# Performance work log

Measured on AMD Instinct MI355X. Metric: run time of the kernel, lower is better.

Reference implementation:

```python
import jax, jax.numpy as jnp
import numpy as np

B, S, D, E = 2, 2048, 1024, 16  # batch, cutoff (seq), dmodel, n_experts


def setup_inputs() -> dict:
    key = jax.random.key(0)
    k = jax.random.split(key, 6)
    scale = 1.0 / np.sqrt(D)
    return {
        "x": jax.random.normal(k[0], (B, S, D), dtype=jnp.float32),
        "gate": jax.random.normal(k[1], (D, E), dtype=jnp.float32) * scale,
        "W1": jax.random.normal(k[2], (E, D, D), dtype=jnp.float32) * scale,  # lin1: Linear(dmodel, dmodel*E), split per expert
        "b1": jnp.zeros((E, D), dtype=jnp.float32),
        "W2": jax.random.normal(k[3], (E, D, D), dtype=jnp.float32) * scale,  # lin2: Linear(dmodel*E, dmodel), split per expert
        "b2": jnp.zeros((D,), dtype=jnp.float32),
        "topk": 256,
    }


def reference(x, gate, W1, b1, W2, b2, topk):
    # Expert-choice gating: softmax over the token (cutoff) axis per expert.
    logits = jnp.einsum("bsd,de->bse", x, gate)            # (B, S, E)
    probs = jax.nn.softmax(logits, axis=1)                  # softmax over tokens
    # Each expert selects its top-k tokens.
    g, idx = jax.lax.top_k(jnp.swapaxes(probs, 1, 2), topk)  # (B, E, k)
    # Gather selected tokens: (B, E, k, D)
    xin = jnp.take_along_axis(x[:, None, :, :], idx[..., None], axis=2)
    # Per-expert 2-layer FFN (hidden size = dmodel, per width = dmodel*n_experts)
    h = jax.nn.relu(jnp.einsum("bekd,edf->bekf", xin, W1) + b1[None, :, None, :])
    out = jnp.einsum("bekf,efd->bekd", h, W2) + b2           # (B, E, k, D)
    weighted = out * g[..., None]
    # Scatter-add back to token positions.
    y = jnp.zeros_like(x)
    b_idx = jnp.arange(x.shape[0])[:, None, None]            # (B, 1, 1)
    y = y.at[b_idx, idx].add(weighted)
    return y
```

## Files before the change

kernel.cpp:

```cpp
#include <hip/hip_runtime.h>
#include <stdint.h>
#include <math.h>

constexpr int CB = 2;
constexpr int CS = 2048;
constexpr int CD = 1024;
constexpr int CE = 16;
constexpr int CK = 256;

typedef short bf16x8 __attribute__((ext_vector_type(8)));
typedef float f32x4 __attribute__((ext_vector_type(4)));

typedef __attribute__((address_space(1))) const unsigned int gu32;
typedef __attribute__((address_space(3))) unsigned int lu32;

__device__ __forceinline__ void async16(const void* g, void* l) {
    __builtin_amdgcn_global_load_lds((gu32*)g, (lu32*)l, 16, 0, 0);
}

__device__ inline unsigned short f2bf(float f) {
    union { float f; uint32_t u; } v; v.f = f;
    uint32_t u = v.u;
    uint32_t r = (u + 0x7FFFu + ((u >> 16) & 1u)) >> 16;
    return (unsigned short)r;
}

__global__ void logits_kernel(const float* __restrict__ x,
                              const float* __restrict__ gate,
                              float* __restrict__ logits) {
    const int bs = blockIdx.x;
    const int l = threadIdx.x;
    const float* xr = x + (size_t)bs * CD;
    float acc[CE];
#pragma unroll
    for (int e = 0; e < CE; e++) acc[e] = 0.0f;
    for (int i = 0; i < CD / 64; i++) {
        const int d = i * 64 + l;
        const float xv = xr[d];
        const float* g = gate + (size_t)d * CE;
#pragma unroll
        for (int e = 0; e < CE; e++) acc[e] += xv * g[e];
    }
#pragma unroll
    for (int e = 0; e < CE; e++) {
        float v = acc[e];
#pragma unroll
        for (int o = 32; o > 0; o >>= 1) v += __shfl_down(v, o);
        if (l == 0) logits[(size_t)bs * CE + e] = v;
    }
}

__global__ void topk_kernel(const float* __restrict__ logits,
                            int* __restrict__ idx_out,
                            float* __restrict__ g_out) {
    const int be = blockIdx.x;
    const int b = be >> 4, e = be & 15;
    const int tid = threadIdx.x;
    const int lane = tid & 63, wid = tid >> 6;

    __shared__ float redf[4];
    __shared__ int hist[256];
    __shared__ int wsum[4];
    __shared__ int sh_bin, sh_rank;
    __shared__ int scnt, eqc;
    __shared__ int eqbuf[CS];

    float lv[8], p[8];
    unsigned int uv[8];
#pragma unroll
    for (int j = 0; j < 8; j++) {
        const int s = tid + j * 256;
        lv[j] = logits[((size_t)(b * CS + s)) * CE + e];
    }
    float m = lv[0];
#pragma unroll
    for (int j = 1; j < 8; j++) m = fmaxf(m, lv[j]);
#pragma unroll
    for (int o = 32; o > 0; o >>= 1) m = fmaxf(m, __shfl_down(m, o));
    if (lane == 0) redf[wid] = m;
    __syncthreads();
    m = fmaxf(fmaxf(redf[0], redf[1]), fmaxf(redf[2], redf[3]));
    __syncthreads();
    float lsum = 0.0f;
#pragma unroll
    for (int j = 0; j < 8; j++) {
        p[j] = expf(lv[j] - m);
        uv[j] = __float_as_uint(p[j]);
        lsum += p[j];
    }
#pragma unroll
    for (int o = 32; o > 0; o >>= 1) lsum += __shfl_down(lsum, o);
    if (lane == 0) redf[wid] = lsum;
    __syncthreads();
    const float total = redf[0] + redf[1] + redf[2] + redf[3];
    const float inv_total = 1.0f / total;

    unsigned int prefix = 0;
    int kneed = CK;
    for (int pass = 0; pass < 4; pass++) {
        const int shift = 24 - 8 * pass;
        __syncthreads();
        hist[tid] = 0;
        __syncthreads();
        const unsigned int hmask = (pass == 0) ? 0u : (0xFFFFFFFFu << (shift + 8));
#pragma unroll
        for (int j = 0; j < 8; j++)
            if ((uv[j] & hmask) == prefix)
                atomicAdd(&hist[(uv[j] >> shift) & 255], 1);
        __syncthreads();
        const int own = hist[tid];
        int s = own;
#pragma unroll
        for (int o = 1; o < 64; o <<= 1) {
            int t = __shfl_down(s, o);
            if (lane + o < 64) s += t;
        }
        if (lane == 0) wsum[wid] = s;
        __syncthreads();
        int above = 0;
        for (int ww = wid + 1; ww < 4; ww++) above += wsum[ww];
        const int incl = s + above;
        if (incl >= kneed && (incl - own) < kneed) {
            sh_bin = tid;
            sh_rank = kneed - (incl - own);
        }
        __syncthreads();
        prefix |= ((unsigned int)sh_bin) << shift;
        kneed = sh_rank;
    }
    const unsigned int v = prefix;
    const int quota = kneed;

    if (tid == 0) { scnt = 0; eqc = 0; }
    __syncthreads();
#pragma unroll
    for (int j = 0; j < 8; j++) {
        const int s = tid + j * 256;
        if (uv[j] > v) {
            const int pos = atomicAdd(&scnt, 1);
            idx_out[be * CK + pos] = s;
            g_out[be * CK + pos] = p[j] * inv_total;
        } else if (uv[j] == v) {
            const int pos = atomicAdd(&eqc, 1);
            eqbuf[pos] = s;
        }
    }
    __syncthreads();
    if (tid == 0) {
        const int cgt = scnt;
        const int n = eqc;
        const float gv = __uint_as_float(v) * inv_total;
        if (n > quota) {
            for (int i = 0; i < quota; i++) {
                int mn = i;
                for (int k2 = i + 1; k2 < n; k2++)
                    if (eqbuf[k2] < eqbuf[mn]) mn = k2;
                const int t2 = eqbuf[i]; eqbuf[i] = eqbuf[mn]; eqbuf[mn] = t2;
            }
        }
        for (int i = 0; i < quota; i++) {
            idx_out[be * CK + cgt + i] = eqbuf[i];
            g_out[be * CK + cgt + i] = gv;
        }
    }
}

__global__ void gather_kernel(const float* __restrict__ x,
                              const int* __restrict__ idx_ws,
                              unsigned short* __restrict__ xinbuf) {
    const int row = blockIdx.x;
    const int be = row >> 8;
    const int b = be >> 4;
    const int tok = idx_ws[row];
    const int c0 = threadIdx.x * 4;
    const f32x4 f = *(const f32x4*)(x + ((size_t)b * CS + tok) * CD + c0);
    union { unsigned short u[4]; uint2 v; } t;
    t.u[0] = f2bf(f[0]); t.u[1] = f2bf(f[1]); t.u[2] = f2bf(f[2]); t.u[3] = f2bf(f[3]);
    *(uint2*)(xinbuf + (size_t)row * CD + c0) = t.v;
}

__global__ __launch_bounds__(256)
void wt_kernel(const float* __restrict__ W, unsigned short* __restrict__ Wt) {
    const int kt = blockIdx.x, nt = blockIdx.y, e = blockIdx.z;
    const float* src = W + (size_t)e * CD * CD;
    unsigned short* dst = Wt + (size_t)e * CD * CD;
    const int tid = threadIdx.x;
    __shared__ unsigned short T[64 * 64];

    const int kr = tid >> 4;
    const int n4 = (tid & 15) << 2;
#pragma unroll
    for (int it = 0; it < 4; it++) {
        const int k = it * 16 + kr;
        const f32x4 v = *(const f32x4*)(src + (size_t)(kt * 64 + k) * CD + nt * 64 + n4);
        const int pp = k >> 4;
        const int klo = k & 15;
#pragma unroll
        for (int i = 0; i < 4; i++) {
            const int n = n4 + i;
            T[n * 64 + ((pp ^ ((n >> 2) & 3)) << 4) + klo] = f2bf(v[i]);
        }
    }
    __syncthreads();
    const int n = tid >> 2;
    const int pp = tid & 3;
    const int sw = pp ^ ((n >> 2) & 3);
    const uint4 a = *(const uint4*)&T[n * 64 + (sw << 4)];
    const uint4 b = *(const uint4*)&T[n * 64 + (sw << 4) + 8];
    unsigned short* drow = dst + (size_t)(nt * 64 + n) * CD + kt * 64 + pp * 16;
    *(uint4*)drow = a;
    *(uint4*)(drow + 8) = b;
}

template <int PHASE>
__global__ __launch_bounds__(256, 2)
void ffn_gemm(const unsigned short* __restrict__ Ain,
              const unsigned short* __restrict__ Wt,
              const float* __restrict__ bias,
              unsigned short* __restrict__ hout,
              const int* __restrict__ idx_ws,
              const float* __restrict__ g_ws,
              float* __restrict__ y) {
    const int mtile = blockIdx.x;
    const int ntile = blockIdx.y;
    const int z = blockIdx.z;
    const int e = z >> 1, b = z & 1;
    const int be = b * 16 + e;
    const int tid = threadIdx.x;
    const int w = tid >> 6, l = tid & 63;
    const int wm = w & 1, wn = w >> 1;
    const int quad = l >> 4, lr = l & 15;

    __shared__ __align__(16) unsigned short As[128 * 32];
    __shared__ __align__(16) unsigned short Bs[128 * 32];

    f32x4 acc[4][4];
    const f32x4 zz = {0.f, 0.f, 0.f, 0.f};
#pragma unroll
    for (int mi = 0; mi < 4; mi++)
#pragma unroll
        for (int ni = 0; ni < 4; ni++) acc[mi][ni] = zz;

    const int sr = l >> 2;
    const int sc = l & 3;
    const unsigned short* Abase = Ain + ((size_t)be * CK + mtile * 128) * CD;
    const unsigned short* Bbase = Wt + ((size_t)e * CD + ntile * 128) * CD;

    for (int k0 = 0; k0 < CD; k0 += 32) {
#pragma unroll
        for (int j = 0; j < 2; j++) {
            const int row = (w * 2 + j) * 16 + sr;
            const size_t goff = (size_t)row * CD + k0 + sc * 8;
            const int loff = (w * 2 + j) * 512 + l * 8;
            async16(Abase + goff, &As[loff]);
            async16(Bbase + goff, &Bs[loff]);
        }
        __syncthreads();

        bf16x8 af[4], bf[4];
#pragma unroll
        for (int mi = 0; mi < 4; mi++)
            af[mi] = *(const bf16x8*)&As[(wm * 64 + mi * 16 + lr) * 32 + quad * 8];
#pragma unroll
        for (int ni = 0; ni < 4; ni++)
            bf[ni] = *(const bf16x8*)&Bs[(wn * 64 + ni * 16 + lr) * 32 + quad * 8];
#pragma unroll
        for (int mi = 0; mi < 4; mi++)
#pragma unroll
            for (int ni = 0; ni < 4; ni++)
                acc[mi][ni] = __builtin_amdgcn_mfma_f32_16x16x32_bf16(
                    af[mi], bf[ni], acc[mi][ni], 0, 0, 0);
        __syncthreads();
    }

    const int gn_base = ntile * 128 + wn * 64;
    if (PHASE == 0) {
#pragma unroll
        for (int mi = 0; mi < 4; mi++)
#pragma unroll
            for (int r = 0; r < 4; r++) {
                const int slot = mtile * 128 + wm * 64 + mi * 16 + quad * 4 + r;
                unsigned short* outrow = hout + ((size_t)be * CK + slot) * CD;
#pragma unroll
                for (int ni = 0; ni < 4; ni++) {
                    const int col = gn_base + ni * 16 + lr;
                    float hv = acc[mi][ni][r] + bias[e * CD + col];
                    hv = fmaxf(hv, 0.0f);
                    outrow[col] = f2bf(hv);
                }
            }
    } else {
#pragma unroll
        for (int mi = 0; mi < 4; mi++)
#pragma unroll
            for (int r = 0; r < 4; r++) {
                const int slot = mtile * 128 + wm * 64 + mi * 16 + quad * 4 + r;
                const int tok = idx_ws[be * CK + slot];
                const float gval = g_ws[be * CK + slot];
                float* yrow = y + ((size_t)b * CS + tok) * CD;
#pragma unroll
                for (int ni = 0; ni < 4; ni++) {
                    const int col = gn_base + ni * 16 + lr;
                    const float val = (acc[mi][ni][r] + bias[col]) * gval;
                    atomicAdd(&yrow[col], val);
                }
            }
    }
}

extern "C" void kernel_launch(void* const* d_in, const int* in_sizes, int n_in,
                              void* d_out, int out_size, void* d_ws, size_t ws_size,
                              hipStream_t stream) {
    const float* x    = (const float*)d_in[0];
    const float* gate = (const float*)d_in[1];
    const float* W1   = (const float*)d_in[2];
    const float* b1   = (const float*)d_in[3];
    const float* W2   = (const float*)d_in[4];
    const float* b2   = (const float*)d_in[5];
    float* y = (float*)d_out;

    char* ws = (char*)d_ws;
    float* logits = (float*)ws;
    int* idxw = (int*)(ws + 262144);
    float* gw = (float*)(ws + 294912);
    unsigned short* xinbuf = (unsigned short*)(ws + 327680);
    unsigned short* hbuf = (unsigned short*)(ws + 17104896);
    unsigned short* wtbuf = (unsigned short*)(ws + 33882112);

    logits_kernel<<<CB * CS, 64, 0, stream>>>(x, gate, logits);
    topk_kernel<<<CB * CE, 256, 0, stream>>>(logits, idxw, gw);
    gather_kernel<<<CB * CE * CK, 256, 0, stream>>>(x, idxw, xinbuf);
    wt_kernel<<<dim3(16, 16, CE), 256, 0, stream>>>(W1, wtbuf);
    hipMemsetAsync(d_out, 0, (size_t)CB * CS * CD * sizeof(float), stream);
    ffn_gemm<0><<<dim3(2, 8, CB * CE), 256, 0, stream>>>(xinbuf, wtbuf, b1, hbuf, idxw, gw, y);
    wt_kernel<<<dim3(16, 16, CE), 256, 0, stream>>>(W2, wtbuf);
    ffn_gemm<1><<<dim3(2, 8, CB * CE), 256, 0, stream>>>(hbuf, wtbuf, b2, nullptr, idxw, gw, y);
}
```

Measured before the change: 302.8 us.

## Retile FFN GEMM to 128x64 with K=64 swizzled LDS, vectorize logits kernel

The FFN GEMM tile shrinks from 128x128 to 128x64 and the K step grows from 32 to 64. This doubles the grid to 1024 blocks and halves the number of barriers per K loop. LDS loads now use an XOR swizzle to avoid bank conflicts, and launch bounds rise to 4 blocks per CU for higher occupancy. The logits kernel packs 4 tokens per 256-thread block and uses vector float4 loads. The cost is less reuse of A per tile and more register pressure under the tighter launch bound.

```diff
diff --git a/kernel.cpp b/kernel.cpp
--- a/kernel.cpp
+++ b/kernel.cpp
@@ -25,21 +25,31 @@
     return (unsigned short)r;
 }
 
-__global__ void logits_kernel(const float* __restrict__ x,
-                              const float* __restrict__ gate,
-                              float* __restrict__ logits) {
-    const int bs = blockIdx.x;
-    const int l = threadIdx.x;
+__global__ __launch_bounds__(256)
+void logits_kernel(const float* __restrict__ x,
+                   const float* __restrict__ gate,
+                   float* __restrict__ logits) {
+    const int tid = threadIdx.x;
+    const int wid = tid >> 6, l = tid & 63;
+    const int bs = blockIdx.x * 4 + wid;
     const float* xr = x + (size_t)bs * CD;
     float acc[CE];
 #pragma unroll
     for (int e = 0; e < CE; e++) acc[e] = 0.0f;
-    for (int i = 0; i < CD / 64; i++) {
-        const int d = i * 64 + l;
-        const float xv = xr[d];
-        const float* g = gate + (size_t)d * CE;
-#pragma unroll
-        for (int e = 0; e < CE; e++) acc[e] += xv * g[e];
+#pragma unroll
+    for (int i = 0; i < 4; i++) {
+        const int d0 = i * 256 + l * 4;
+        const f32x4 xv = *(const f32x4*)(xr + d0);
+#pragma unroll
+        for (int j = 0; j < 4; j++) {
+            const f32x4* g4 = (const f32x4*)(gate + (size_t)(d0 + j) * CE);
+#pragma unroll
+            for (int c = 0; c < 4; c++) {
+                const f32x4 gv = g4[c];
+#pragma unroll
+                for (int u = 0; u < 4; u++) acc[c * 4 + u] += xv[j] * gv[u];
+            }
+        }
     }
 #pragma unroll
     for (int e = 0; e < CE; e++) {
@@ -213,7 +223,7 @@
 }
 
 template <int PHASE>
-__global__ __launch_bounds__(256, 2)
+__global__ __launch_bounds__(256, 4)
 void ffn_gemm(const unsigned short* __restrict__ Ain,
               const unsigned short* __restrict__ Wt,
               const float* __restrict__ bias,
@@ -231,49 +241,57 @@
     const int wm = w & 1, wn = w >> 1;
     const int quad = l >> 4, lr = l & 15;
 
-    __shared__ __align__(16) unsigned short As[128 * 32];
-    __shared__ __align__(16) unsigned short Bs[128 * 32];
-
-    f32x4 acc[4][4];
+    __shared__ __align__(16) unsigned short As[128 * 64];
+    __shared__ __align__(16) unsigned short Bs[64 * 64];
+
+    f32x4 acc[4][2];
     const f32x4 zz = {0.f, 0.f, 0.f, 0.f};
 #pragma unroll
     for (int mi = 0; mi < 4; mi++)
 #pragma unroll
-        for (int ni = 0; ni < 4; ni++) acc[mi][ni] = zz;
-
-    const int sr = l >> 2;
-    const int sc = l & 3;
+        for (int ni = 0; ni < 2; ni++) acc[mi][ni] = zz;
+
     const unsigned short* Abase = Ain + ((size_t)be * CK + mtile * 128) * CD;
-    const unsigned short* Bbase = Wt + ((size_t)e * CD + ntile * 128) * CD;
-
-    for (int k0 = 0; k0 < CD; k0 += 32) {
+    const unsigned short* Bbase = Wt + ((size_t)e * CD + ntile * 64) * CD;
+
+    for (int k0 = 0; k0 < CD; k0 += 64) {
+#pragma unroll
+        for (int j = 0; j < 4; j++) {
+            const int c = (w * 4 + j) * 64 + l;
+            const int row = c >> 3;
+            const int q = (c & 7) ^ (row & 7);
+            async16(Abase + (size_t)row * CD + k0 + q * 8, &As[c * 8]);
+        }
 #pragma unroll
         for (int j = 0; j < 2; j++) {
-            const int row = (w * 2 + j) * 16 + sr;
-            const size_t goff = (size_t)row * CD + k0 + sc * 8;
-            const int loff = (w * 2 + j) * 512 + l * 8;
-            async16(Abase + goff, &As[loff]);
-            async16(Bbase + goff, &Bs[loff]);
-        }
-        __syncthreads();
-
-        bf16x8 af[4], bf[4];
-#pragma unroll
-        for (int mi = 0; mi < 4; mi++)
-            af[mi] = *(const bf16x8*)&As[(wm * 64 + mi * 16 + lr) * 32 + quad * 8];
-#pragma unroll
-        for (int ni = 0; ni < 4; ni++)
-            bf[ni] = *(const bf16x8*)&Bs[(wn * 64 + ni * 16 + lr) * 32 + quad * 8];
-#pragma unroll
-        for (int mi = 0; mi < 4; mi++)
-#pragma unroll
-            for (int ni = 0; ni < 4; ni++)
-                acc[mi][ni] = __builtin_amdgcn_mfma_f32_16x16x32_bf16(
-                    af[mi], bf[ni], acc[mi][ni], 0, 0, 0);
-        __syncthreads();
-    }
-
-    const int gn_base = ntile * 128 + wn * 64;
+            const int c = (w * 2 + j) * 64 + l;
+            const int row = c >> 3;
+            const int q = (c & 7) ^ (row & 7);
+            async16(Bbase + (size_t)row * CD + k0 + q * 8, &Bs[c * 8]);
+        }
+        __syncthreads();
+
+#pragma unroll
+        for (int kk = 0; kk < 2; kk++) {
+            bf16x8 af[4], bfr[2];
+            const int sq = ((kk * 4 + quad) ^ (lr & 7)) * 8;
+#pragma unroll
+            for (int mi = 0; mi < 4; mi++)
+                af[mi] = *(const bf16x8*)&As[(wm * 64 + mi * 16 + lr) * 64 + sq];
+#pragma unroll
+            for (int ni = 0; ni < 2; ni++)
+                bfr[ni] = *(const bf16x8*)&Bs[(wn * 32 + ni * 16 + lr) * 64 + sq];
+#pragma unroll
+            for (int mi = 0; mi < 4; mi++)
+#pragma unroll
+                for (int ni = 0; ni < 2; ni++)
+                    acc[mi][ni] = __builtin_amdgcn_mfma_f32_16x16x32_bf16(
+                        af[mi], bfr[ni], acc[mi][ni], 0, 0, 0);
+        }
+        __syncthreads();
+    }
+
+    const int gn_base = ntile * 64 + wn * 32;
     if (PHASE == 0) {
 #pragma unroll
         for (int mi = 0; mi < 4; mi++)
@@ -282,7 +300,7 @@
                 const int slot = mtile * 128 + wm * 64 + mi * 16 + quad * 4 + r;
                 unsigned short* outrow = hout + ((size_t)be * CK + slot) * CD;
 #pragma unroll
-                for (int ni = 0; ni < 4; ni++) {
+                for (int ni = 0; ni < 2; ni++) {
                     const int col = gn_base + ni * 16 + lr;
                     float hv = acc[mi][ni][r] + bias[e * CD + col];
                     hv = fmaxf(hv, 0.0f);
@@ -299,7 +317,7 @@
                 const float gval = g_ws[be * CK + slot];
                 float* yrow = y + ((size_t)b * CS + tok) * CD;
 #pragma unroll
-                for (int ni = 0; ni < 4; ni++) {
+                for (int ni = 0; ni < 2; ni++) {
                     const int col = gn_base + ni * 16 + lr;
                     const float val = (acc[mi][ni][r] + bias[col]) * gval;
                     atomicAdd(&yrow[col], val);
@@ -327,12 +345,12 @@
     unsigned short* hbuf = (unsigned short*)(ws + 17104896);
     unsigned short* wtbuf = (unsigned short*)(ws + 33882112);
 
-    logits_kernel<<<CB * CS, 64, 0, stream>>>(x, gate, logits);
+    logits_kernel<<<CB * CS / 4, 256, 0, stream>>>(x, gate, logits);
     topk_kernel<<<CB * CE, 256, 0, stream>>>(logits, idxw, gw);
     gather_kernel<<<CB * CE * CK, 256, 0, stream>>>(x, idxw, xinbuf);
     wt_kernel<<<dim3(16, 16, CE), 256, 0, stream>>>(W1, wtbuf);
     hipMemsetAsync(d_out, 0, (size_t)CB * CS * CD * sizeof(float), stream);
-    ffn_gemm<0><<<dim3(2, 8, CB * CE), 256, 0, stream>>>(xinbuf, wtbuf, b1, hbuf, idxw, gw, y);
+    ffn_gemm<0><<<dim3(2, 16, CB * CE), 256, 0, stream>>>(xinbuf, wtbuf, b1, hbuf, idxw, gw, y);
     wt_kernel<<<dim3(16, 16, CE), 256, 0, stream>>>(W2, wtbuf);
-    ffn_gemm<1><<<dim3(2, 8, CB * CE), 256, 0, stream>>>(hbuf, wtbuf, b2, nullptr, idxw, gw, y);
-}
+    ffn_gemm<1><<<dim3(2, 16, CB * CE), 256, 0, stream>>>(hbuf, wtbuf, b2, nullptr, idxw, gw, y);
+}
```

Result: slower. 316.3 us (+4.5%).
